# Kernel tuning notes

Measured on AMD Instinct MI355X. Metric: run time of the kernel, lower is better.

The kernel has to match this reference:

```python
import jax, jax.numpy as jnp
from jax import lax
import numpy as np

K = 3          # kernel_size
PAD = 1        # K // 2
MAX_OFFSET = 0.1
EPS = 1e-8


def setup_inputs() -> dict:
    key = jax.random.key(0)
    k0, k1, k2 = jax.random.split(key, 3)
    B, C, H, W = 4, 64, 256, 256
    Cmid = C // 4
    x = jax.random.normal(k0, (B, C, H, W), jnp.float32)
    # offset_predictor: Conv2d(C+9, C//4, 3, pad=1) -> LeakyReLU(0.2) -> Conv2d(C//4, 2, 3, pad=1) -> Tanh
    w1 = jax.random.normal(k1, (Cmid, C + K * K, 3, 3), jnp.float32) * 0.05
    b1 = jnp.zeros((Cmid,), jnp.float32)
    w2 = jax.random.normal(k2, (2, Cmid, 3, 3), jnp.float32) * 0.05
    b2 = jnp.zeros((2,), jnp.float32)
    return {"x": x, "w1": w1, "b1": b1, "w2": w2, "b2": b2}


def _conv2d(x, w, b):
    # NCHW, OIHW, stride 1, pad 1 (SAME for 3x3)
    out = lax.conv_general_dilated(x, w, (1, 1), ((PAD, PAD), (PAD, PAD)),
                                   dimension_numbers=("NCHW", "OIHW", "NCHW"))
    return out + b[None, :, None, None]


def _local_cosine_similarity(x):
    # F.unfold with zero padding: neighbors[k] at spatial shift (di-1, dj-1), row-major k = di*K + dj
    B, C, H, W = x.shape
    xp = jnp.pad(x, ((0, 0), (0, 0), (PAD, PAD), (PAD, PAD)))
    neighbors = jnp.stack([xp[:, :, di:di + H, dj:dj + W]
                           for di in range(K) for dj in range(K)], axis=2)  # (B,C,9,H,W)
    center = x[:, :, None, :, :]                                            # (B,C,1,H,W)
    numerator = jnp.sum(neighbors * center, axis=1)                         # (B,9,H,W)
    center_norm = jnp.sqrt(jnp.sum(x * x, axis=1)) + EPS                    # (B,H,W)
    neighbor_norm = jnp.sqrt(jnp.sum(neighbors * neighbors, axis=1)) + EPS  # (B,9,H,W)
    return numerator / (center_norm[:, None] * neighbor_norm)               # (B,9,H,W)


def _grid_sample_border(x, grid):
    # bilinear, padding_mode='border', align_corners=True; grid: (B,H,W,2) with (gx,gy) in [-1,1]
    B, C, H, W = x.shape
    ix = (grid[..., 0] + 1.0) * 0.5 * (W - 1)
    iy = (grid[..., 1] + 1.0) * 0.5 * (H - 1)
    ix = jnp.clip(ix, 0.0, W - 1)
    iy = jnp.clip(iy, 0.0, H - 1)
    x0f = jnp.floor(ix); y0f = jnp.floor(iy)
    wx = ix - x0f; wy = iy - y0f
    x0 = x0f.astype(jnp.int32); y0 = y0f.astype(jnp.int32)
    x1 = jnp.minimum(x0 + 1, W - 1); y1 = jnp.minimum(y0 + 1, H - 1)

    def gather(img, yy, xx):  # img (C,H,W), yy/xx (H,W) -> (C,H,W)
        return img[:, yy, xx]

    g = jax.vmap(gather)
    v00 = g(x, y0, x0); v01 = g(x, y0, x1)
    v10 = g(x, y1, x0); v11 = g(x, y1, x1)
    wx = wx[:, None]; wy = wy[:, None]  # broadcast over channel dim
    return ((1 - wy) * ((1 - wx) * v00 + wx * v01)
            + wy * ((1 - wx) * v10 + wx * v11))


def reference(x, w1, b1, w2, b2):
    B, C, H, W = x.shape
    sim = _local_cosine_similarity(x)                       # (B,9,H,W)
    features = jnp.concatenate([x, sim], axis=1)            # (B,C+9,H,W)
    h = _conv2d(features, w1, b1)
    h = jnp.where(h >= 0, h, 0.2 * h)                       # LeakyReLU(0.2)
    offset = jnp.tanh(_conv2d(h, w2, b2)) * MAX_OFFSET      # (B,2,H,W)
    gy, gx = jnp.meshgrid(jnp.linspace(-1.0, 1.0, H),
                          jnp.linspace(-1.0, 1.0, W), indexing="ij")
    base_grid = jnp.stack([gx, gy], axis=-1)[None]          # (1,H,W,2)
    offset_grid = base_grid + jnp.transpose(offset, (0, 2, 3, 1))
    return _grid_sample_border(x, offset_grid)
```

## Files before the change

### kernel.cpp

```cpp
#include <hip/hip_runtime.h>
#include <math.h>

#define B 4
#define C 64
#define H 256
#define W 256
#define CMID 16
#define CIN 73
#define HW (H*W)
#define NW (CIN*9*CMID)
#define XS_STRIDE 260
#define PLN 258
#define SE  258

__global__ void transpose_w1_kernel(const float* __restrict__ w1, float* __restrict__ wt) {
    int tid = blockIdx.x * blockDim.x + threadIdx.x;
    if (tid >= NW) return;
    int co = tid & (CMID - 1);
    int rest = tid >> 4;
    int ci = rest / 9;
    int k = rest - ci * 9;
    wt[tid] = w1[(co * CIN + ci) * 9 + k];
}

__global__ __launch_bounds__(256) void sim_kernel(const float* __restrict__ x,
                                                  float* __restrict__ sim) {
    __shared__ float xs[2][4][4 * SE];

    int bid = blockIdx.x;
    int sb = (bid & 7) * 64 + (bid >> 3);
    int b  = sb >> 7;
    int y0 = (sb & 127) << 1;
    int tid = threadIdx.x;
    int rl = tid >> 7;
    int k  = tid & 127;
    int px = k << 1;
    int y  = y0 + rl;

    int scol = (tid & 1) ? 130 + (tid >> 1) : (tid >> 1);

    bool rv[4];
    size_t off[4];
#pragma unroll
    for (int j = 0; j < 4; ++j) {
        int grow = y0 - 1 + j;
        rv[j] = (grow >= 0) && (grow < H);
        off[j] = (size_t)grow * W + tid;
    }

    if (tid < 64) {
        int e = tid & 1;
        int r = (tid >> 1) & 3;
        int q = tid >> 3;
        (&xs[0][0][0])[q * (4 * SE) + r * SE + 128 + e] = 0.f;
    }

    float dot0[9], nsq0[9], dot1[9], nsq1[9];
    float csq0 = 0.f, csq1 = 0.f;
#pragma unroll
    for (int i = 0; i < 9; ++i) { dot0[i] = dot1[i] = nsq0[i] = nsq1[i] = 0.f; }

    const float* xb = x + (size_t)b * C * HW;
    float p[16];
#pragma unroll
    for (int kk = 0; kk < 4; ++kk)
#pragma unroll
        for (int j = 0; j < 4; ++j)
            p[kk * 4 + j] = rv[j] ? xb[(size_t)kk * HW + off[j]] : 0.f;

    int cur = 0;
#pragma unroll 1
    for (int cc = 0; cc < C; cc += 4) {
#pragma unroll
        for (int kk = 0; kk < 4; ++kk)
#pragma unroll
            for (int j = 0; j < 4; ++j)
                xs[cur][kk][j * SE + scol] = p[kk * 4 + j];
        __syncthreads();

        if (cc + 4 < C) {
#pragma unroll
            for (int kk = 0; kk < 4; ++kk)
#pragma unroll
                for (int j = 0; j < 4; ++j)
                    p[kk * 4 + j] = rv[j] ? xb[(size_t)(cc + 4 + kk) * HW + off[j]] : 0.f;
        }

#pragma unroll
        for (int kk = 0; kk < 4; ++kk) {
            const float* base = &xs[cur][kk][rl * SE];
            float v[3][4];
#pragma unroll
            for (int r = 0; r < 3; ++r) {
                const float* rp = base + r * SE;
                v[r][0] = rp[129 + k];
                v[r][1] = rp[k];
                v[r][2] = rp[130 + k];
                v[r][3] = rp[k + 1];
            }
            float cv0 = v[1][1], cv1 = v[1][2];
            csq0 = fmaf(cv0, cv0, csq0);
            csq1 = fmaf(cv1, cv1, csq1);
#pragma unroll
            for (int kr = 0; kr < 3; ++kr)
#pragma unroll
                for (int kc = 0; kc < 3; ++kc) {
                    int kk9 = kr * 3 + kc;
                    if (kk9 == 4) continue;
                    float n0 = v[kr][kc], n1 = v[kr][kc + 1];
                    dot0[kk9] = fmaf(cv0, n0, dot0[kk9]);
                    nsq0[kk9] = fmaf(n0, n0, nsq0[kk9]);
                    dot1[kk9] = fmaf(cv1, n1, dot1[kk9]);
                    nsq1[kk9] = fmaf(n1, n1, nsq1[kk9]);
                }
        }
        cur ^= 1;
    }

    dot0[4] = csq0; nsq0[4] = csq0;
    dot1[4] = csq1; nsq1[4] = csq1;
    float cn0 = sqrtf(csq0) + 1e-8f;
    float cn1 = sqrtf(csq1) + 1e-8f;
    float* so = sim + (size_t)b * 9 * HW + (size_t)y * W + px;
#pragma unroll
    for (int kk9 = 0; kk9 < 9; ++kk9) {
        float s0 = dot0[kk9] / (cn0 * (sqrtf(nsq0[kk9]) + 1e-8f));
        float s1 = dot1[kk9] / (cn1 * (sqrtf(nsq1[kk9]) + 1e-8f));
        *(float2*)(so + (size_t)kk9 * HW) = make_float2(s0, s1);
    }
}

__device__ __forceinline__ void conv1_co4(const float* __restrict__ pl, int l,
                                          int aL, int aR,
                                          const float4 wv[9], float4 acc[2][4]) {
    float v[4][6];
#pragma unroll
    for (int r = 0; r < 4; ++r) {
        const float* rp = pl + r * PLN;
        v[r][1] = rp[l];
        v[r][2] = rp[64 + l];
        v[r][3] = rp[128 + l];
        v[r][4] = rp[192 + l];
        v[r][0] = rp[aL];
        v[r][5] = rp[aR];
    }
#pragma unroll
    for (int kr = 0; kr < 3; ++kr)
#pragma unroll
        for (int kc = 0; kc < 3; ++kc) {
            float4 w = wv[kr * 3 + kc];
#pragma unroll
            for (int rr = 0; rr < 2; ++rr)
#pragma unroll
                for (int cc = 0; cc < 4; ++cc) {
                    float a = v[rr + kr][cc + kc];
                    acc[rr][cc].x = fmaf(a, w.x, acc[rr][cc].x);
                    acc[rr][cc].y = fmaf(a, w.y, acc[rr][cc].y);
                    acc[rr][cc].z = fmaf(a, w.z, acc[rr][cc].z);
                    acc[rr][cc].w = fmaf(a, w.w, acc[rr][cc].w);
                }
        }
}

__global__ __launch_bounds__(256) void conv1_kernel(const float* __restrict__ x,
                                                    const float* __restrict__ sim,
                                                    const float* __restrict__ wt,
                                                    const float* __restrict__ b1,
                                                    float* __restrict__ h) {
    __shared__ float xs[2][2][4 * PLN];

    int tid = threadIdx.x;
    int l = tid & 63;
    int wid = tid >> 6;
    int bid = blockIdx.x;
    int sb = (bid & 7) * 64 + (bid >> 3);
    int b  = sb >> 7;
    int y0 = (sb & 127) << 1;

    int vz;
    asm volatile("v_mov_b32 %0, 0" : "=v"(vz));
    const float4* wq = (const float4*)wt + vz;

    const float* gx = x + (size_t)b * C * HW;
    const float* gs = sim + (size_t)b * 9 * HW;

    int grow = y0 - 1 + wid;
    bool rvw = (grow >= 0) && (grow < H);
    size_t goff = (size_t)grow * W + 4 * l;

    int aL = (l == 0)  ? 256 : 191 + l;
    int aR = (l == 63) ? 257 : l + 1;

    if (tid < 32) {
        int bu = tid >> 4, ch = (tid >> 3) & 1, r = (tid >> 1) & 3, e = tid & 1;
        xs[bu][ch][r * PLN + 256 + e] = 0.f;
    }

    float4 bias = ((const float4*)b1)[wid];
    float4 acc[2][4];
#pragma unroll
    for (int rr = 0; rr < 2; ++rr)
#pragma unroll
        for (int cc = 0; cc < 4; ++cc) acc[rr][cc] = bias;

    float4 wA[9], wB[9];
#pragma unroll
    for (int k = 0; k < 9; ++k) wA[k] = wq[k * 4 + wid];

    const float4 z4 = make_float4(0.f, 0.f, 0.f, 0.f);
    float4 p0 = z4, p1 = z4;
    if (rvw) {
        p0 = *(const float4*)(gx + goff);
        p1 = *(const float4*)(gx + HW + goff);
    }

    int cur = 0;
#pragma unroll 1
    for (int cc2 = 0; cc2 < 72; cc2 += 2) {
        {
            float* d0 = &xs[cur][0][wid * PLN];
            d0[l] = p0.x; d0[64 + l] = p0.y; d0[128 + l] = p0.z; d0[192 + l] = p0.w;
            float* d1 = &xs[cur][1][wid * PLN];
            d1[l] = p1.x; d1[64 + l] = p1.y; d1[128 + l] = p1.z; d1[192 + l] = p1.w;
        }
        __syncthreads();

        {
            int ci = cc2 + 2;
            p0 = z4;
            if (rvw)
                p0 = (ci < C) ? *(const float4*)(gx + (size_t)ci * HW + goff)
                              : *(const float4*)(gs + (size_t)(ci - C) * HW + goff);
            int cj = cc2 + 3;
            p1 = z4;
            if (rvw && cj < CIN)
                p1 = (cj < C) ? *(const float4*)(gx + (size_t)cj * HW + goff)
                              : *(const float4*)(gs + (size_t)(cj - C) * HW + goff);
        }

#pragma unroll
        for (int k = 0; k < 9; ++k) wB[k] = wq[((cc2 + 1) * 9 + k) * 4 + wid];

        conv1_co4(&xs[cur][0][0], l, aL, aR, wA, acc);

#pragma unroll
        for (int k = 0; k < 9; ++k) wA[k] = wq[((cc2 + 2) * 9 + k) * 4 + wid];

        conv1_co4(&xs[cur][1][0], l, aL, aR, wB, acc);

        cur ^= 1;
    }

    {
        float* d0 = &xs[cur][0][wid * PLN];
        d0[l] = p0.x; d0[64 + l] = p0.y; d0[128 + l] = p0.z; d0[192 + l] = p0.w;
    }
    __syncthreads();
    conv1_co4(&xs[cur][0][0], l, aL, aR, wA, acc);

    float* ho = h + ((size_t)b * CMID + 4 * wid) * HW + (size_t)y0 * W + 4 * l;
#pragma unroll
    for (int rr = 0; rr < 2; ++rr)
#pragma unroll
        for (int j = 0; j < 4; ++j) {
            float4 o;
            o.x = ((const float*)&acc[rr][0])[j];
            o.y = ((const float*)&acc[rr][1])[j];
            o.z = ((const float*)&acc[rr][2])[j];
            o.w = ((const float*)&acc[rr][3])[j];
            o.x = o.x >= 0.f ? o.x : 0.2f * o.x;
            o.y = o.y >= 0.f ? o.y : 0.2f * o.y;
            o.z = o.z >= 0.f ? o.z : 0.2f * o.z;
            o.w = o.w >= 0.f ? o.w : 0.2f * o.w;
            *(float4*)(ho + (size_t)j * HW + (size_t)rr * W) = o;
        }
}

__device__ __forceinline__ void read_patch_lds(const float* __restrict__ xsbuf,
                                               int rl, int px, float v[3][4]) {
    const float* pb = xsbuf + rl * XS_STRIDE + px;
#pragma unroll
    for (int r = 0; r < 3; ++r) {
        float2 p0 = *(const float2*)(pb + r * XS_STRIDE);
        float2 p1 = *(const float2*)(pb + r * XS_STRIDE + 2);
        v[r][0] = p0.x; v[r][1] = p0.y; v[r][2] = p1.x; v[r][3] = p1.y;
    }
}

__global__ __launch_bounds__(256) void offset_kernel(const float* __restrict__ h,
                                                     const float* __restrict__ w2,
                                                     const float* __restrict__ b2,
                                                     float2* __restrict__ off_buf) {
    __shared__ float lw2[CMID * 9 * 2];
    __shared__ float xs[2][4][4 * XS_STRIDE];

    int tid = threadIdx.x;
    for (int i = tid; i < CMID * 9 * 2; i += 256) {
        int co = i & 1;
        int rest = i >> 1;
        int ci = rest / 9;
        int kk = rest - ci * 9;
        lw2[i] = w2[(co * CMID + ci) * 9 + kk];
    }

    int bid = blockIdx.x;
    int sb = (bid & 7) * 64 + (bid >> 3);
    int b  = sb >> 7;
    int y0 = (sb & 127) << 1;
    int srow = tid >> 6;
    int sx4  = (tid & 63) << 2;
    int rl = tid >> 7;
    int px = (tid & 127) << 1;
    int y  = y0 + rl;

    int grow = y0 - 1 + srow;
    bool gvalid = (grow >= 0) && (grow < H);
    const float* gh = h + (size_t)b * CMID * HW + (size_t)grow * W + sx4;

    if (tid < 64) {
        int bu = tid >> 5, ch = (tid >> 3) & 3, r = (tid >> 1) & 3;
        int e = (tid & 1) ? 257 : 0;
        xs[bu][ch][r * XS_STRIDE + e] = 0.f;
    }

    float s0x = b2[0], s0y = b2[1], s1x = b2[0], s1y = b2[1];

    const float4 z4 = make_float4(0.f, 0.f, 0.f, 0.f);
    float4 pr[4];
#pragma unroll
    for (int k = 0; k < 4; ++k)
        pr[k] = gvalid ? *(const float4*)(gh + (size_t)k * HW) : z4;

    int cur = 0;
#pragma unroll 1
    for (int cg4 = 0; cg4 < CMID; cg4 += 4) {
#pragma unroll
        for (int k = 0; k < 4; ++k) {
            float* dst = &xs[cur][k][srow * XS_STRIDE + 1 + sx4];
            dst[0] = pr[k].x; dst[1] = pr[k].y; dst[2] = pr[k].z; dst[3] = pr[k].w;
        }
        __syncthreads();

        if (cg4 + 4 < CMID) {
#pragma unroll
            for (int k = 0; k < 4; ++k)
                pr[k] = gvalid ? *(const float4*)(gh + (size_t)(cg4 + 4 + k) * HW) : z4;
        }

#pragma unroll
        for (int k = 0; k < 4; ++k) {
            float v[3][4];
            read_patch_lds(xs[cur][k], rl, px, v);
            int ci = cg4 + k;
#pragma unroll
            for (int kr = 0; kr < 3; ++kr)
#pragma unroll
                for (int kc = 0; kc < 3; ++kc) {
                    float2 wv = *(const float2*)(lw2 + (ci * 9 + kr * 3 + kc) * 2);
                    s0x = fmaf(v[kr][kc],     wv.x, s0x);
                    s0y = fmaf(v[kr][kc],     wv.y, s0y);
                    s1x = fmaf(v[kr][kc + 1], wv.x, s1x);
                    s1y = fmaf(v[kr][kc + 1], wv.y, s1y);
                }
        }
        cur ^= 1;
    }

    float ix0 = (float)px       + 0.1f * tanhf(s0x) * (0.5f * (float)(W - 1));
    float iy0 = (float)y        + 0.1f * tanhf(s0y) * (0.5f * (float)(H - 1));
    float ix1 = (float)(px + 1) + 0.1f * tanhf(s1x) * (0.5f * (float)(W - 1));
    float iy1 = (float)y        + 0.1f * tanhf(s1y) * (0.5f * (float)(H - 1));
    ix0 = fminf(fmaxf(ix0, 0.f), (float)(W - 1));
    iy0 = fminf(fmaxf(iy0, 0.f), (float)(H - 1));
    ix1 = fminf(fmaxf(ix1, 0.f), (float)(W - 1));
    iy1 = fminf(fmaxf(iy1, 0.f), (float)(H - 1));

    float4* op = (float4*)(off_buf + (size_t)b * HW + (size_t)y * W + px);
    *op = make_float4(ix0, iy0, ix1, iy1);
}

#define SROWS 35
__global__ __launch_bounds__(256) void sample_kernel(const float* __restrict__ x,
                                                     const float2* __restrict__ off_buf,
                                                     float* __restrict__ out) {
    __shared__ float xs[SROWS * 256 + 2];

    int bid = blockIdx.x;
    int sb = (bid & 7) * 16 + (bid >> 3);
    int b  = sb >> 5;
    int ty = sb & 31;
    int cg = blockIdx.y;
    int tid = threadIdx.x;

    int ybase = ty << 3;
    int lo = ybase - 13;

    int a00[8], a10[8];
    float wx[8], wy[8];
    const float2* ob2 = off_buf + (size_t)b * HW + (size_t)ybase * W + tid;
#pragma unroll
    for (int r = 0; r < 8; ++r) {
        float2 o = ob2[r * W];
        float xf = floorf(o.x), yf = floorf(o.y);
        wx[r] = o.x - xf; wy[r] = o.y - yf;
        int x0 = (int)xf, yy0 = (int)yf;
        int yy1 = min(yy0 + 1, H - 1);
        a00[r] = ((yy0 - lo) << 8) + x0;
        a10[r] = ((yy1 - lo) << 8) + x0;
    }

    if (tid < 2) xs[SROWS * 256 + tid] = 0.f;

    const float* xb = x + ((size_t)b * C + cg * 4) * HW;
    float* outb = out + ((size_t)b * C + cg * 4) * HW + (size_t)ybase * W + tid;

#pragma unroll 1
    for (int c = 0; c < 4; ++c) {
        __syncthreads();
        const float* src = xb + (size_t)c * HW;
        for (int j = tid; j < SROWS * 64; j += 256) {
            int row = j >> 6, x4 = (j & 63) << 2;
            int grw = min(max(lo + row, 0), H - 1);
            *(float4*)&xs[(row << 8) + x4] = *(const float4*)(src + (size_t)grw * W + x4);
        }
        __syncthreads();
        float* oc = outb + (size_t)c * HW;
#pragma unroll
        for (int r = 0; r < 8; ++r) {
            float t0 = xs[a00[r]], t1 = xs[a00[r] + 1];
            float b0 = xs[a10[r]], b1 = xs[a10[r] + 1];
            float top = fmaf(wx[r], t1 - t0, t0);
            float bot = fmaf(wx[r], b1 - b0, b0);
            oc[r * W] = fmaf(wy[r], bot - top, top);
        }
    }
}

extern "C" void kernel_launch(void* const* d_in, const int* in_sizes, int n_in,
                              void* d_out, int out_size, void* d_ws, size_t ws_size,
                              hipStream_t stream) {
    const float* x  = (const float*)d_in[0];
    const float* w1 = (const float*)d_in[1];
    const float* b1 = (const float*)d_in[2];
    const float* w2 = (const float*)d_in[3];
    const float* b2 = (const float*)d_in[4];
    float* out = (float*)d_out;

    float* ws  = (float*)d_ws;
    float* wt  = ws;
    float* sim = ws + 16384;
    float* h   = sim + (size_t)B * 9 * HW;
    float2* off_buf = (float2*)(h + (size_t)B * CMID * HW);

    transpose_w1_kernel<<<(NW + 255) / 256, 256, 0, stream>>>(w1, wt);

    sim_kernel<<<512, 256, 0, stream>>>(x, sim);
    conv1_kernel<<<512, 256, 0, stream>>>(x, sim, wt, b1, h);
    offset_kernel<<<512, 256, 0, stream>>>(h, w2, b2, off_buf);
    sample_kernel<<<dim3(128, 16), 256, 0, stream>>>(x, off_buf, out);
}
```

Measured before the change: 239.8 us.

## Split conv1 input channels across two blocks and fuse w1 transpose into sim kernel

Measured after the change: 248.7 us. 1.04x slower.

```diff
diff --git a/kernel.cpp b/kernel.cpp
--- a/kernel.cpp
+++ b/kernel.cpp
@@ -13,25 +13,29 @@
 #define PLN 258
 #define SE  258
 
-__global__ void transpose_w1_kernel(const float* __restrict__ w1, float* __restrict__ wt) {
-    int tid = blockIdx.x * blockDim.x + threadIdx.x;
-    if (tid >= NW) return;
-    int co = tid & (CMID - 1);
-    int rest = tid >> 4;
-    int ci = rest / 9;
-    int k = rest - ci * 9;
-    wt[tid] = w1[(co * CIN + ci) * 9 + k];
-}
-
 __global__ __launch_bounds__(256) void sim_kernel(const float* __restrict__ x,
-                                                  float* __restrict__ sim) {
+                                                  float* __restrict__ sim,
+                                                  const float* __restrict__ w1,
+                                                  float* __restrict__ wt) {
     __shared__ float xs[2][4][4 * SE];
 
     int bid = blockIdx.x;
+    int tid = threadIdx.x;
+
+    {
+        int gidx = bid * 256 + tid;
+        if (gidx < NW) {
+            int co = gidx & (CMID - 1);
+            int rest = gidx >> 4;
+            int ci = rest / 9;
+            int k = rest - ci * 9;
+            wt[gidx] = w1[(co * CIN + ci) * 9 + k];
+        }
+    }
+
     int sb = (bid & 7) * 64 + (bid >> 3);
     int b  = sb >> 7;
     int y0 = (sb & 127) << 1;
-    int tid = threadIdx.x;
     int rl = tid >> 7;
     int k  = tid & 127;
     int px = k << 1;
@@ -166,16 +170,22 @@
                                                     const float* __restrict__ sim,
                                                     const float* __restrict__ wt,
                                                     const float* __restrict__ b1,
-                                                    float* __restrict__ h) {
+                                                    float* __restrict__ hp0,
+                                                    float* __restrict__ hp1) {
     __shared__ float xs[2][2][4 * PLN];
 
     int tid = threadIdx.x;
     int l = tid & 63;
     int wid = tid >> 6;
     int bid = blockIdx.x;
-    int sb = (bid & 7) * 64 + (bid >> 3);
+    int half = bid & 1;
+    int inner = bid >> 1;
+    int sb = (inner & 7) * 64 + (inner >> 3);
     int b  = sb >> 7;
     int y0 = (sb & 127) << 1;
+
+    int cstart = half ? 36 : 0;
+    int climit = half ? 73 : 36;
 
     int vz;
     asm volatile("v_mov_b32 %0, 0" : "=v"(vz));
@@ -196,27 +206,29 @@
         xs[bu][ch][r * PLN + 256 + e] = 0.f;
     }
 
-    float4 bias = ((const float4*)b1)[wid];
+    const float4 z4 = make_float4(0.f, 0.f, 0.f, 0.f);
     float4 acc[2][4];
-#pragma unroll
-    for (int rr = 0; rr < 2; ++rr)
-#pragma unroll
-        for (int cc = 0; cc < 4; ++cc) acc[rr][cc] = bias;
+    {
+        float4 init = half ? z4 : ((const float4*)b1)[wid];
+#pragma unroll
+        for (int rr = 0; rr < 2; ++rr)
+#pragma unroll
+            for (int cc = 0; cc < 4; ++cc) acc[rr][cc] = init;
+    }
 
     float4 wA[9], wB[9];
 #pragma unroll
-    for (int k = 0; k < 9; ++k) wA[k] = wq[k * 4 + wid];
-
-    const float4 z4 = make_float4(0.f, 0.f, 0.f, 0.f);
+    for (int k = 0; k < 9; ++k) wA[k] = wq[(cstart * 9 + k) * 4 + wid];
+
     float4 p0 = z4, p1 = z4;
     if (rvw) {
-        p0 = *(const float4*)(gx + goff);
-        p1 = *(const float4*)(gx + HW + goff);
+        p0 = *(const float4*)(gx + (size_t)cstart * HW + goff);
+        p1 = *(const float4*)(gx + (size_t)(cstart + 1) * HW + goff);
     }
 
     int cur = 0;
 #pragma unroll 1
-    for (int cc2 = 0; cc2 < 72; cc2 += 2) {
+    for (int cc2 = cstart; cc2 < cstart + 36; cc2 += 2) {
         {
             float* d0 = &xs[cur][0][wid * PLN];
             d0[l] = p0.x; d0[64 + l] = p0.y; d0[128 + l] = p0.z; d0[192 + l] = p0.w;
@@ -228,12 +240,12 @@
         {
             int ci = cc2 + 2;
             p0 = z4;
-            if (rvw)
+            if (rvw && ci < climit)
                 p0 = (ci < C) ? *(const float4*)(gx + (size_t)ci * HW + goff)
                               : *(const float4*)(gs + (size_t)(ci - C) * HW + goff);
             int cj = cc2 + 3;
             p1 = z4;
-            if (rvw && cj < CIN)
+            if (rvw && cj < climit)
                 p1 = (cj < C) ? *(const float4*)(gx + (size_t)cj * HW + goff)
                               : *(const float4*)(gs + (size_t)(cj - C) * HW + goff);
         }
@@ -251,14 +263,15 @@
         cur ^= 1;
     }
 
-    {
+    if (half) {
         float* d0 = &xs[cur][0][wid * PLN];
         d0[l] = p0.x; d0[64 + l] = p0.y; d0[128 + l] = p0.z; d0[192 + l] = p0.w;
-    }
-    __syncthreads();
-    conv1_co4(&xs[cur][0][0], l, aL, aR, wA, acc);
-
-    float* ho = h + ((size_t)b * CMID + 4 * wid) * HW + (size_t)y0 * W + 4 * l;
+        __syncthreads();
+        conv1_co4(&xs[cur][0][0], l, aL, aR, wA, acc);
+    }
+
+    float* hp = half ? hp1 : hp0;
+    float* ho = hp + ((size_t)b * CMID + 4 * wid) * HW + (size_t)y0 * W + 4 * l;
 #pragma unroll
     for (int rr = 0; rr < 2; ++rr)
 #pragma unroll
@@ -268,10 +281,6 @@
             o.y = ((const float*)&acc[rr][1])[j];
             o.z = ((const float*)&acc[rr][2])[j];
             o.w = ((const float*)&acc[rr][3])[j];
-            o.x = o.x >= 0.f ? o.x : 0.2f * o.x;
-            o.y = o.y >= 0.f ? o.y : 0.2f * o.y;
-            o.z = o.z >= 0.f ? o.z : 0.2f * o.z;
-            o.w = o.w >= 0.f ? o.w : 0.2f * o.w;
             *(float4*)(ho + (size_t)j * HW + (size_t)rr * W) = o;
         }
 }
@@ -287,7 +296,8 @@
     }
 }
 
-__global__ __launch_bounds__(256) void offset_kernel(const float* __restrict__ h,
+__global__ __launch_bounds__(256) void offset_kernel(const float* __restrict__ hp0,
+                                                     const float* __restrict__ hp1,
                                                      const float* __restrict__ w2,
                                                      const float* __restrict__ b2,
                                                      float2* __restrict__ off_buf) {
@@ -315,7 +325,9 @@
 
     int grow = y0 - 1 + srow;
     bool gvalid = (grow >= 0) && (grow < H);
-    const float* gh = h + (size_t)b * CMID * HW + (size_t)grow * W + sx4;
+    size_t hoff = (size_t)b * CMID * HW + (size_t)grow * W + sx4;
+    const float* gh0 = hp0 + hoff;
+    const float* gh1 = hp1 + hoff;
 
     if (tid < 64) {
         int bu = tid >> 5, ch = (tid >> 3) & 3, r = (tid >> 1) & 3;
@@ -326,25 +338,36 @@
     float s0x = b2[0], s0y = b2[1], s1x = b2[0], s1y = b2[1];
 
     const float4 z4 = make_float4(0.f, 0.f, 0.f, 0.f);
-    float4 pr[4];
-#pragma unroll
-    for (int k = 0; k < 4; ++k)
-        pr[k] = gvalid ? *(const float4*)(gh + (size_t)k * HW) : z4;
+    float4 pa[4], pb[4];
+#pragma unroll
+    for (int k = 0; k < 4; ++k) {
+        pa[k] = gvalid ? *(const float4*)(gh0 + (size_t)k * HW) : z4;
+        pb[k] = gvalid ? *(const float4*)(gh1 + (size_t)k * HW) : z4;
+    }
 
     int cur = 0;
 #pragma unroll 1
     for (int cg4 = 0; cg4 < CMID; cg4 += 4) {
 #pragma unroll
         for (int k = 0; k < 4; ++k) {
+            float4 s;
+            s.x = pa[k].x + pb[k].x; s.y = pa[k].y + pb[k].y;
+            s.z = pa[k].z + pb[k].z; s.w = pa[k].w + pb[k].w;
+            s.x = s.x >= 0.f ? s.x : 0.2f * s.x;
+            s.y = s.y >= 0.f ? s.y : 0.2f * s.y;
+            s.z = s.z >= 0.f ? s.z : 0.2f * s.z;
+            s.w = s.w >= 0.f ? s.w : 0.2f * s.w;
             float* dst = &xs[cur][k][srow * XS_STRIDE + 1 + sx4];
-            dst[0] = pr[k].x; dst[1] = pr[k].y; dst[2] = pr[k].z; dst[3] = pr[k].w;
+            dst[0] = s.x; dst[1] = s.y; dst[2] = s.z; dst[3] = s.w;
         }
         __syncthreads();
 
         if (cg4 + 4 < CMID) {
 #pragma unroll
-            for (int k = 0; k < 4; ++k)
-                pr[k] = gvalid ? *(const float4*)(gh + (size_t)(cg4 + 4 + k) * HW) : z4;
+            for (int k = 0; k < 4; ++k) {
+                pa[k] = gvalid ? *(const float4*)(gh0 + (size_t)(cg4 + 4 + k) * HW) : z4;
+                pb[k] = gvalid ? *(const float4*)(gh1 + (size_t)(cg4 + 4 + k) * HW) : z4;
+            }
         }
 
 #pragma unroll
@@ -449,13 +472,12 @@
     float* ws  = (float*)d_ws;
     float* wt  = ws;
     float* sim = ws + 16384;
-    float* h   = sim + (size_t)B * 9 * HW;
-    float2* off_buf = (float2*)(h + (size_t)B * CMID * HW);
-
-    transpose_w1_kernel<<<(NW + 255) / 256, 256, 0, stream>>>(w1, wt);
-
-    sim_kernel<<<512, 256, 0, stream>>>(x, sim);
-    conv1_kernel<<<512, 256, 0, stream>>>(x, sim, wt, b1, h);
-    offset_kernel<<<512, 256, 0, stream>>>(h, w2, b2, off_buf);
+    float* hp0 = sim + (size_t)B * 9 * HW;
+    float2* off_buf = (float2*)(hp0 + (size_t)B * CMID * HW);
+    float* hp1 = (float*)(off_buf + (size_t)B * HW);
+
+    sim_kernel<<<512, 256, 0, stream>>>(x, sim, w1, wt);
+    conv1_kernel<<<1024, 256, 0, stream>>>(x, sim, wt, b1, hp0, hp1);
+    offset_kernel<<<512, 256, 0, stream>>>(hp0, hp1, w2, b2, off_buf);
     sample_kernel<<<dim3(128, 16), 256, 0, stream>>>(x, off_buf, out);
 }
```
